# Kernel tuning notes

Hardware: AMD Instinct MI355X
Metric: run time of the kernel (lower is better)

## Reference

```python
import jax, jax.numpy as jnp
import numpy as np

N_NODES = 50000
N_EDGES = 800000
N_GRAPHS = 1024
BN_EPS = 1e-5

def _linear_params(key, fan_in, fan_out):
    k1, k2 = jax.random.split(key)
    lim = 1.0 / np.sqrt(fan_in)
    w = jax.random.uniform(k1, (fan_in, fan_out), jnp.float32, -lim, lim)
    b = jax.random.uniform(k2, (fan_out,), jnp.float32, -lim, lim)
    return w, b


def setup_inputs() -> dict:
    key = jax.random.key(0)
    ks = jax.random.split(key, 16)
    x = jax.random.normal(ks[0], (N_NODES, 114), jnp.float32)
    edge_index = jax.random.randint(ks[1], (2, N_EDGES), 0, N_NODES, jnp.int64)
    batch = jnp.sort(jax.random.randint(ks[2], (N_NODES,), 0, N_GRAPHS, jnp.int64))
    w1a, b1a = _linear_params(ks[3], 114, 198)
    w1b, b1b = _linear_params(ks[4], 198, 198)
    w2a, b2a = _linear_params(ks[5], 198, 64)
    w2b, b2b = _linear_params(ks[6], 64, 64)
    w3a, b3a = _linear_params(ks[7], 64, 32)
    w3b, b3b = _linear_params(ks[8], 32, 32)
    fw1, fb1 = _linear_params(ks[9], 32, 16)
    fw2, fb2 = _linear_params(ks[10], 16, 8)
    ow, ob = _linear_params(ks[11], 8, 2)
    g1 = jnp.ones((198,), jnp.float32); be1 = jnp.zeros((198,), jnp.float32)
    g2 = jnp.ones((64,), jnp.float32); be2 = jnp.zeros((64,), jnp.float32)
    g3 = jnp.ones((32,), jnp.float32); be3 = jnp.zeros((32,), jnp.float32)
    return dict(x=x, edge_index=edge_index, batch=batch,
                w1a=w1a, b1a=b1a, w1b=w1b, b1b=b1b, g1=g1, be1=be1,
                w2a=w2a, b2a=b2a, w2b=w2b, b2b=b2b, g2=g2, be2=be2,
                w3a=w3a, b3a=b3a, w3b=w3b, b3b=b3b, g3=g3, be3=be3,
                fw1=fw1, fb1=fb1, fw2=fw2, fb2=fb2, ow=ow, ob=ob)


def _gin_conv(x, src, dst, wa, ba, wb, bb):
    # GINConv, eps=0: h_i = MLP((1+eps)*x_i + sum_{j->i} x_j)
    agg = jax.ops.segment_sum(x[src], dst, num_segments=N_NODES)
    h = x + agg
    h = jax.nn.relu(h @ wa + ba) @ wb + bb
    return h


def _batchnorm(h, gamma, beta):
    # training-mode BN over the node axis (biased variance, as torch)
    mean = jnp.mean(h, axis=0)
    var = jnp.var(h, axis=0)
    return (h - mean) * jax.lax.rsqrt(var + BN_EPS) * gamma + beta


def reference(x, edge_index, batch,
              w1a, b1a, w1b, b1b, g1, be1,
              w2a, b2a, w2b, b2b, g2, be2,
              w3a, b3a, w3b, b3b, g3, be3,
              fw1, fb1, fw2, fb2, ow, ob):
    src, dst = edge_index[0], edge_index[1]
    h = jax.nn.relu(_gin_conv(x, src, dst, w1a, b1a, w1b, b1b))
    h = _batchnorm(h, g1, be1)
    h = jax.nn.relu(_gin_conv(h, src, dst, w2a, b2a, w2b, b2b))
    h = _batchnorm(h, g2, be2)
    h = jax.nn.relu(_gin_conv(h, src, dst, w3a, b3a, w3b, b3b))
    h = _batchnorm(h, g3, be3)
    g = jax.ops.segment_sum(h, batch, num_segments=N_GRAPHS)  # global_add_pool
    g = jax.nn.relu(g @ fw1 + fb1)
    g = jax.nn.relu(g @ fw2 + fb2)
    return g @ ow + ob
```

## Files before the change

kernel.cpp:

```cpp
#include <hip/hip_runtime.h>

#define NODES  50000
#define EDGES  800000
#define GRAPHS 1024
#define P      200

#define SCAN_BLK 256
#define SCAN_NB  ((NODES + SCAN_BLK - 1) / SCAN_BLK)

typedef __attribute__((ext_vector_type(8))) short short8v;
typedef __attribute__((ext_vector_type(4))) short short4v;
typedef __attribute__((ext_vector_type(4))) float f32x4;

__device__ __forceinline__ ushort f2bf(float f) {
    uint u = __float_as_uint(f);
    u = u + 0x7FFFu + ((u >> 16) & 1u);
    return (ushort)(u >> 16);
}

__global__ void hist_kernel(const int* __restrict__ dst, int* __restrict__ deg,
                            const int* __restrict__ batch, int* __restrict__ cnt) {
    int e = blockIdx.x * blockDim.x + threadIdx.x;
    if (e < EDGES) atomicAdd(&deg[dst[e]], 1);
    if (e < NODES) atomicAdd(&cnt[batch[e]], 1);
}

__global__ void scan_part(const int* __restrict__ deg, int* __restrict__ part) {
    __shared__ int sh[SCAN_BLK];
    int t = threadIdx.x;
    int n = blockIdx.x * SCAN_BLK + t;
    sh[t] = (n < NODES) ? deg[n] : 0;
    __syncthreads();
    for (int off = SCAN_BLK / 2; off > 0; off >>= 1) {
        if (t < off) sh[t] += sh[t + off];
        __syncthreads();
    }
    if (t == 0) part[blockIdx.x] = sh[0];
}

__global__ void scan_scan(int* __restrict__ part) {
    __shared__ int sh[SCAN_BLK];
    int t = threadIdx.x;
    int v = (t < SCAN_NB) ? part[t] : 0;
    sh[t] = v;
    __syncthreads();
    for (int off = 1; off < SCAN_BLK; off <<= 1) {
        int u = 0;
        if (t >= off) u = sh[t - off];
        __syncthreads();
        if (t >= off) sh[t] += u;
        __syncthreads();
    }
    if (t < SCAN_NB) part[t] = sh[t] - v;
}

__global__ void scan_expand(const int* __restrict__ deg, const int* __restrict__ part,
                            int* __restrict__ rowstart, int* __restrict__ cursor) {
    __shared__ int sh[SCAN_BLK];
    int t = threadIdx.x;
    int n = blockIdx.x * SCAN_BLK + t;
    int v = (n < NODES) ? deg[n] : 0;
    sh[t] = v;
    __syncthreads();
    for (int off = 1; off < SCAN_BLK; off <<= 1) {
        int u = 0;
        if (t >= off) u = sh[t - off];
        __syncthreads();
        if (t >= off) sh[t] += u;
        __syncthreads();
    }
    int excl = sh[t] - v + part[blockIdx.x];
    if (n < NODES) {
        rowstart[n] = excl;
        cursor[n]   = excl;
        if (n == NODES - 1) rowstart[NODES] = excl + v;
    }
}

__global__ void scatter_kernel(const int* __restrict__ src, const int* __restrict__ dst,
                               int* __restrict__ cursor, int* __restrict__ csrc) {
    int e = blockIdx.x * blockDim.x + threadIdx.x;
    if (e < EDGES) {
        int p = atomicAdd(&cursor[dst[e]], 1);
        csrc[p] = src[e];
    }
}

__global__ void pad_all(const float* __restrict__ w1a, const float* __restrict__ w1b,
                        const float* __restrict__ w2a, const float* __restrict__ w2b,
                        const float* __restrict__ w3a, const float* __restrict__ w3b,
                        ushort* __restrict__ WF1, ushort* __restrict__ WF2,
                        ushort* __restrict__ WF3, ushort* __restrict__ WF4,
                        ushort* __restrict__ WF5, ushort* __restrict__ WF6) {
    int s = blockIdx.x * blockDim.x + threadIdx.x;
    const float* W; ushort* out; int K, N, NCH, CT, base;
    if      (s < 65536)  { W = w1a; out = WF1; K = 114; N = 198; NCH = 4; CT = 16; base = 0; }
    else if (s < 180224) { W = w1b; out = WF2; K = 198; N = 198; NCH = 7; CT = 16; base = 65536; }
    else if (s < 208896) { W = w2a; out = WF3; K = 198; N = 64;  NCH = 7; CT = 4;  base = 180224; }
    else if (s < 217088) { W = w2b; out = WF4; K = 64;  N = 64;  NCH = 2; CT = 4;  base = 208896; }
    else if (s < 225280) { W = w3a; out = WF5; K = 64;  N = 32;  NCH = 2; CT = 4;  base = 217088; }
    else if (s < 229376) { W = w3b; out = WF6; K = 32;  N = 32;  NCH = 1; CT = 4;  base = 225280; }
    else return;
    int idx = s - base;
    int half = NCH * CT * 512;
    int h = idx / half, r = idx % half;
    int j = r & 7, col = (r >> 3) & 15, kg = (r >> 7) & 3;
    int rest = r >> 9;
    int ct = rest % CT, c = rest / CT;
    int k = c * 32 + kg * 8 + j;
    int n = ct * 16 + col;
    float v = (k < K && n < N) ? W[k * N + n] : 0.0f;
    ushort hi = f2bf(v);
    if (h == 0) out[idx] = hi;
    else {
        float hf = __uint_as_float(((uint)hi) << 16);
        out[idx] = f2bf(v - hf);
    }
}

template<int D>
__global__ void csr_agg(const float* __restrict__ feat, int fpitch,
                        const int* __restrict__ rowstart, const int* __restrict__ csrc,
                        float* __restrict__ agg, int opitch) {
    int wid  = (blockIdx.x * blockDim.x + threadIdx.x) >> 6;
    int lane = threadIdx.x & 63;
    if (wid >= NODES) return;
    const int r0 = rowstart[wid], r1 = rowstart[wid + 1];
    constexpr int UNR = 8;
    if constexpr (D == 114) {
        const bool act = lane < 57;
        float sx = 0.0f, sy = 0.0f;
        for (int base = r0; base < r1; base += 64) {
            const int myidx = (base + lane < r1) ? csrc[base + lane] : 0;
            const int cnt = min(64, r1 - base);
            int t = 0;
            for (; t + UNR <= cnt; t += UNR) {
                const float2* p[UNR];
#pragma unroll
                for (int u = 0; u < UNR; u++)
                    p[u] = (const float2*)(feat + (size_t)__shfl(myidx, t + u) * fpitch);
                float2 v[UNR];
#pragma unroll
                for (int u = 0; u < UNR; u++) if (act) v[u] = p[u][lane];
                if (act) {
                    float ax = 0.0f, ay = 0.0f;
#pragma unroll
                    for (int u = 0; u < UNR; u++) { ax += v[u].x; ay += v[u].y; }
                    sx += ax; sy += ay;
                }
            }
            for (; t < cnt; t++) {
                const float2* fp2 = (const float2*)(feat + (size_t)__shfl(myidx, t) * fpitch);
                if (act) { float2 v = fp2[lane]; sx += v.x; sy += v.y; }
            }
        }
        if (act) *(float2*)(agg + (size_t)wid * opitch + 2 * lane) = make_float2(sx, sy);
    } else {
        float s = 0.0f;
        for (int base = r0; base < r1; base += 64) {
            const int myidx = (base + lane < r1) ? csrc[base + lane] : 0;
            const int cnt = min(64, r1 - base);
            int t = 0;
            for (; t + UNR <= cnt; t += UNR) {
                const float* p[UNR];
#pragma unroll
                for (int u = 0; u < UNR; u++)
                    p[u] = feat + (size_t)__shfl(myidx, t + u) * fpitch;
                float v[UNR];
#pragma unroll
                for (int u = 0; u < UNR; u++)
                    if (lane < D) v[u] = p[u][lane];
                if (lane < D) {
                    float acc = 0.0f;
#pragma unroll
                    for (int u = 0; u < UNR; u++) acc += v[u];
                    s += acc;
                }
            }
            for (; t < cnt; t++) {
                const float* fp2 = feat + (size_t)__shfl(myidx, t) * fpitch;
                if (lane < D) s += fp2[lane];
            }
        }
        if (lane < D) agg[(size_t)wid * opitch + lane] = s;
    }
}

__launch_bounds__(256)
__global__ void gemm_fused_l1(const float* __restrict__ X,
                              const float* __restrict__ A2,
                              const ushort* __restrict__ WF1,
                              const float* __restrict__ B1,
                              const ushort* __restrict__ WF2,
                              const float* __restrict__ B2,
                              float* __restrict__ OUT,
                              float* __restrict__ gsum, float* __restrict__ gsq) {
    constexpr int K1   = 114;
    constexpr int NCH1 = 4;
    constexpr int NCH2 = 7;
    constexpr int CT   = 16;
    constexpr int CTW  = 4;
    constexpr int NN   = 198;

    __shared__ __align__(16) ushort A_lds[2][2][2][4][16][8];
    __shared__ __align__(16) ushort M_lds[2][NCH2][2][4][16][8];
    __shared__ float shSum[256];
    __shared__ float shSq [256];

    const int tid  = threadIdx.x;
    const int lane = tid & 63;
    const int wv   = tid >> 6;
    const int node0 = blockIdx.x * 32;

    for (int n = tid; n < 256; n += 256) { shSum[n] = 0.0f; shSq[n] = 0.0f; }

    const int sr  = tid >> 3;
    const int sc4 = (tid & 7) * 4;
    const int skg = sc4 >> 3;
    const int sj0 = sc4 & 7;
    const int gn  = node0 + sr;
    const size_t fstride1 = (size_t)NCH1 * CT * 512;
    const size_t fstride2 = (size_t)NCH2 * CT * 512;

    float xv[4];
    float a2v[4];

    auto loadA = [&](int c) {
        const int k0 = c * 32 + sc4;
#pragma unroll
        for (int j = 0; j < 4; j++) {
            int gk = k0 + j;
            bool ok = (gn < NODES && gk < K1);
            xv[j]  = ok ? X[(size_t)gn * K1 + gk] : 0.0f;
            a2v[j] = ok ? A2[(size_t)gn * P + gk] : 0.0f;
        }
    };
    auto cvtStore = [&](int buf, int c) {
        const int k0 = c * 32 + sc4;
        short4v hv, lv;
#pragma unroll
        for (int j = 0; j < 4; j++) {
            int gk = k0 + j;
            float t = 0.0f;
            if (gn < NODES && gk < K1) t = xv[j] + a2v[j];
            ushort h = f2bf(t);
            float hf = __uint_as_float(((uint)h) << 16);
            ushort l = f2bf(t - hf);
            hv[j] = (short)h; lv[j] = (short)l;
        }
        *(short4v*)&A_lds[buf][0][sr >> 4][skg][sr & 15][sj0] = hv;
        *(short4v*)&A_lds[buf][1][sr >> 4][skg][sr & 15][sj0] = lv;
    };

    f32x4 acc1[2][CTW] = {};
    loadA(0);
    cvtStore(0, 0);
    __syncthreads();

    const int kg = lane >> 4, rw = lane & 15;
#pragma unroll
    for (int c = 0; c < NCH1; c++) {
        const int buf = c & 1;
        if (c + 1 < NCH1) loadA(c + 1);

        short8v ah[2], al[2];
#pragma unroll
        for (int rt = 0; rt < 2; rt++) {
            ah[rt] = *(const short8v*)&A_lds[buf][0][rt][kg][rw][0];
            al[rt] = *(const short8v*)&A_lds[buf][1][rt][kg][rw][0];
        }
        const size_t fb0 = ((size_t)(c * CT + wv * CTW)) * 512 + (size_t)lane * 8;
        short8v wh = *(const short8v*)(WF1 + fb0);
        short8v wl = *(const short8v*)(WF1 + fstride1 + fb0);
#pragma unroll
        for (int t = 0; t < CTW; t++) {
            short8v nwh, nwl;
            if (t + 1 < CTW) {
                const size_t fb = fb0 + (size_t)(t + 1) * 512;
                nwh = *(const short8v*)(WF1 + fb);
                nwl = *(const short8v*)(WF1 + fstride1 + fb);
            }
            __builtin_amdgcn_s_setprio(1);
#pragma unroll
            for (int rt = 0; rt < 2; rt++) {
                acc1[rt][t] = __builtin_amdgcn_mfma_f32_16x16x32_bf16(ah[rt], wh, acc1[rt][t], 0, 0, 0);
                acc1[rt][t] = __builtin_amdgcn_mfma_f32_16x16x32_bf16(al[rt], wh, acc1[rt][t], 0, 0, 0);
                acc1[rt][t] = __builtin_amdgcn_mfma_f32_16x16x32_bf16(ah[rt], wl, acc1[rt][t], 0, 0, 0);
            }
            __builtin_amdgcn_s_setprio(0);
            if (t + 1 < CTW) { wh = nwh; wl = nwl; }
        }
        if (c + 1 < NCH1) cvtStore((c + 1) & 1, c + 1);
        __syncthreads();
    }

    const int mg = lane >> 4, colb = lane & 15;
#pragma unroll
    for (int t = 0; t < CTW; t++) {
        const int ct = wv * CTW + t;
        if (ct >= 14) continue;
        const int n = ct * 16 + colb;
        const float bn = (n < NN) ? B1[n] : 0.0f;
        const int c2 = n >> 5, kg2 = (n >> 3) & 3, j2 = n & 7;
#pragma unroll
        for (int rt = 0; rt < 2; rt++) {
#pragma unroll
            for (int j = 0; j < 4; j++) {
                float vv = fmaxf(acc1[rt][t][j] + bn, 0.0f);
                if (n >= NN) vv = 0.0f;
                ushort h = f2bf(vv);
                float hf = __uint_as_float(((uint)h) << 16);
                ushort l = f2bf(vv - hf);
                int row = mg * 4 + j;
                M_lds[0][c2][rt][kg2][row][j2] = h;
                M_lds[1][c2][rt][kg2][row][j2] = l;
            }
        }
    }
    __syncthreads();

    f32x4 acc2[2][CTW] = {};
#pragma unroll
    for (int c = 0; c < NCH2; c++) {
        short8v ah[2], al[2];
#pragma unroll
        for (int rt = 0; rt < 2; rt++) {
            ah[rt] = *(const short8v*)&M_lds[0][c][rt][kg][rw][0];
            al[rt] = *(const short8v*)&M_lds[1][c][rt][kg][rw][0];
        }
        const size_t fb0 = ((size_t)(c * CT + wv * CTW)) * 512 + (size_t)lane * 8;
        short8v wh = *(const short8v*)(WF2 + fb0);
        short8v wl = *(const short8v*)(WF2 + fstride2 + fb0);
#pragma unroll
        for (int t = 0; t < CTW; t++) {
            short8v nwh, nwl;
            if (t + 1 < CTW) {
                const size_t fb = fb0 + (size_t)(t + 1) * 512;
                nwh = *(const short8v*)(WF2 + fb);
                nwl = *(const short8v*)(WF2 + fstride2 + fb);
            }
            __builtin_amdgcn_s_setprio(1);
#pragma unroll
            for (int rt = 0; rt < 2; rt++) {
                acc2[rt][t] = __builtin_amdgcn_mfma_f32_16x16x32_bf16(ah[rt], wh, acc2[rt][t], 0, 0, 0);
                acc2[rt][t] = __builtin_amdgcn_mfma_f32_16x16x32_bf16(al[rt], wh, acc2[rt][t], 0, 0, 0);
                acc2[rt][t] = __builtin_amdgcn_mfma_f32_16x16x32_bf16(ah[rt], wl, acc2[rt][t], 0, 0, 0);
            }
            __builtin_amdgcn_s_setprio(0);
            if (t + 1 < CTW) { wh = nwh; wl = nwl; }
        }
    }

#pragma unroll
    for (int t = 0; t < CTW; t++) {
        const int ct = wv * CTW + t;
        const int n = ct * 16 + colb;
        const float bn = (n < NN) ? B2[n] : 0.0f;
        float psum = 0.0f, psq = 0.0f;
#pragma unroll
        for (int rt = 0; rt < 2; rt++) {
#pragma unroll
            for (int j = 0; j < 4; j++) {
                int m = node0 + rt * 16 + mg * 4 + j;
                float vv = fmaxf(acc2[rt][t][j] + bn, 0.0f);
                if (m < NODES && n < NN) {
                    OUT[(size_t)m * P + n] = vv;
                    psum += vv; psq += vv * vv;
                }
            }
        }
        if (n < NN) {
            atomicAdd(&shSum[n], psum);
            atomicAdd(&shSq[n], psq);
        }
    }
    __syncthreads();
    for (int n = tid; n < NN; n += 256) {
        atomicAdd(&gsum[n], shSum[n]);
        atomicAdd(&gsq[n], shSq[n]);
    }
}

template<int K, int N, bool ADD2, bool STATS, bool BNX, bool PRE, bool ACT,
         bool WRITE, bool POOL>
__launch_bounds__(256)
__global__ void gemm_mfma(const float* __restrict__ X, int xpitch,
                          const float* __restrict__ A2, int apitch,
                          const ushort* __restrict__ WF,
                          const float* __restrict__ B,
                          const float* __restrict__ PREB,
                          const float* __restrict__ scale, const float* __restrict__ shift,
                          float* __restrict__ OUT, int opitch,
                          float* __restrict__ gsum, float* __restrict__ gsq,
                          const int* __restrict__ batch, float* __restrict__ gpool) {
    constexpr int KP  = ((K + 31) / 32) * 32;
    constexpr int NCH = KP / 32;
    constexpr int NP  = ((N + 63) / 64) * 64;
    constexpr int CT  = NP / 16;
    constexpr int CTW = CT / 4;
    static_assert(CT % 4 == 0, "col tiles must split across 4 waves");

    __shared__ __align__(16) ushort A_lds[2][2][2][4][16][8];
    __shared__ float shSum[STATS ? NP : 4];
    __shared__ float shSq [STATS ? NP : 4];

    const int tid  = threadIdx.x;
    const int lane = tid & 63;
    const int wv   = tid >> 6;
    const int node0 = blockIdx.x * 32;

    if (STATS) {
        for (int n = tid; n < NP; n += 256) { shSum[n] = 0.0f; shSq[n] = 0.0f; }
    }

    f32x4 acc[2][CTW] = {};

    const int sr  = tid >> 3;
    const int sc4 = (tid & 7) * 4;
    const int skg = sc4 >> 3;
    const int sj0 = sc4 & 7;
    const int gn  = node0 + sr;
    const size_t fstride = (size_t)NCH * CT * 512;

    float xvA[4], xvB[4];
    float a2vA[ADD2 ? 4 : 1], a2vB[ADD2 ? 4 : 1];

    auto loadA_A = [&](int c) {
        const int k0 = c * 32 + sc4;
#pragma unroll
        for (int j = 0; j < 4; j++) {
            int gk = k0 + j;
            bool ok = (gn < NODES && gk < K);
            xvA[j] = ok ? X[(size_t)gn * xpitch + gk] : 0.0f;
            if (ADD2) a2vA[j] = ok ? A2[(size_t)gn * apitch + gk] : 0.0f;
        }
    };
    auto loadA_B = [&](int c) {
        const int k0 = c * 32 + sc4;
#pragma unroll
        for (int j = 0; j < 4; j++) {
            int gk = k0 + j;
            bool ok = (gn < NODES && gk < K);
            xvB[j] = ok ? X[(size_t)gn * xpitch + gk] : 0.0f;
            if (ADD2) a2vB[j] = ok ? A2[(size_t)gn * apitch + gk] : 0.0f;
        }
    };
    auto cvtCore = [&](int buf, int c, const float* xv, const float* a2v) {
        const int k0 = c * 32 + sc4;
        short4v hv, lv;
#pragma unroll
        for (int j = 0; j < 4; j++) {
            int gk = k0 + j;
            float t = 0.0f;
            if (gn < NODES && gk < K) {
                t = xv[j];
                if (BNX) t = fmaf(t, scale[gk], shift[gk]);
                if (ADD2) t += a2v[j];
                if (PRE)  t = fmaxf(t + PREB[gk], 0.0f);
            }
            ushort h = f2bf(t);
            float hf = __uint_as_float(((uint)h) << 16);
            ushort l = f2bf(t - hf);
            hv[j] = (short)h; lv[j] = (short)l;
        }
        *(short4v*)&A_lds[buf][0][sr >> 4][skg][sr & 15][sj0] = hv;
        *(short4v*)&A_lds[buf][1][sr >> 4][skg][sr & 15][sj0] = lv;
    };

    loadA_A(0);
    if (NCH > 1) loadA_B(1);
    cvtCore(0, 0, xvA, ADD2 ? a2vA : xvA);
    __syncthreads();

    const int kg = lane >> 4, rw = lane & 15;
#pragma unroll
    for (int c = 0; c < NCH; c++) {
        const int buf = c & 1;
        if (c + 2 < NCH) {
            if ((c & 1) == 0) loadA_A(c + 2);
            else              loadA_B(c + 2);
        }

        short8v ah[2], al[2];
#pragma unroll
        for (int rt = 0; rt < 2; rt++) {
            ah[rt] = *(const short8v*)&A_lds[buf][0][rt][kg][rw][0];
            al[rt] = *(const short8v*)&A_lds[buf][1][rt][kg][rw][0];
        }

        const size_t fb0 = ((size_t)(c * CT + wv * CTW)) * 512 + (size_t)lane * 8;
        short8v wh = *(const short8v*)(WF + fb0);
        short8v wl = *(const short8v*)(WF + fstride + fb0);
#pragma unroll
        for (int t = 0; t < CTW; t++) {
            short8v nwh, nwl;
            if (t + 1 < CTW) {
                const size_t fb = fb0 + (size_t)(t + 1) * 512;
                nwh = *(const short8v*)(WF + fb);
                nwl = *(const short8v*)(WF + fstride + fb);
            }
            __builtin_amdgcn_s_setprio(1);
#pragma unroll
            for (int rt = 0; rt < 2; rt++) {
                acc[rt][t] = __builtin_amdgcn_mfma_f32_16x16x32_bf16(ah[rt], wh, acc[rt][t], 0, 0, 0);
                acc[rt][t] = __builtin_amdgcn_mfma_f32_16x16x32_bf16(al[rt], wh, acc[rt][t], 0, 0, 0);
                acc[rt][t] = __builtin_amdgcn_mfma_f32_16x16x32_bf16(ah[rt], wl, acc[rt][t], 0, 0, 0);
            }
            __builtin_amdgcn_s_setprio(0);
            if (t + 1 < CTW) { wh = nwh; wl = nwl; }
        }

        if (c + 1 < NCH) {
            if (((c + 1) & 1) == 0) cvtCore((c + 1) & 1, c + 1, xvA, ADD2 ? a2vA : xvA);
            else                    cvtCore((c + 1) & 1, c + 1, xvB, ADD2 ? a2vB : xvB);
        }
        __syncthreads();
    }

    const int mg = lane >> 4, colb = lane & 15;
#pragma unroll
    for (int t = 0; t < CTW; t++) {
        const int ct = wv * CTW + t;
        const int n = ct * 16 + colb;
        const float bn = (ACT && n < N) ? B[n] : 0.0f;
        float psum = 0.0f, psq = 0.0f;
#pragma unroll
        for (int rt = 0; rt < 2; rt++) {
#pragma unroll
            for (int j = 0; j < 4; j++) {
                int m = node0 + rt * 16 + mg * 4 + j;
                float vv = ACT ? fmaxf(acc[rt][t][j] + bn, 0.0f) : acc[rt][t][j];
                if (m < NODES && n < N) {
                    if (WRITE) OUT[(size_t)m * opitch + n] = vv;
                    if (STATS) { psum += vv; psq += vv * vv; }
                    if (POOL)  atomicAdd(&gpool[batch[m] * 32 + n], vv);
                }
            }
        }
        if (STATS && n < N) {
            atomicAdd(&shSum[n], psum);
            atomicAdd(&shSq[n], psq);
        }
    }
    if (STATS) {
        __syncthreads();
        for (int n = tid; n < N; n += 256) {
            atomicAdd(&gsum[n], shSum[n]);
            atomicAdd(&gsq[n], shSq[n]);
        }
    }
}

template<int N>
__global__ void bn_finalize(const float* __restrict__ sum, const float* __restrict__ sq,
                            const float* __restrict__ gamma, const float* __restrict__ beta,
                            float* __restrict__ scale, float* __restrict__ shift) {
    int n = threadIdx.x;
    if (n < N) {
        float mean = sum[n] * (1.0f / NODES);
        float var  = sq[n] * (1.0f / NODES) - mean * mean;
        var = var < 0.0f ? 0.0f : var;
        float sc = gamma[n] * rsqrtf(var + 1e-5f);
        scale[n] = sc;
        shift[n] = beta[n] - mean * sc;
    }
}

__global__ void head_kernel(const float* __restrict__ graw, const int* __restrict__ cnt,
                            const float* __restrict__ scale, const float* __restrict__ shift,
                            const float* __restrict__ fw1, const float* __restrict__ fb1,
                            const float* __restrict__ fw2, const float* __restrict__ fb2,
                            const float* __restrict__ ow, const float* __restrict__ ob,
                            float* __restrict__ out) {
    int gi = blockIdx.x * blockDim.x + threadIdx.x;
    if (gi >= GRAPHS) return;
    float cf = (float)cnt[gi];
    float v[32];
#pragma unroll
    for (int k = 0; k < 32; k++)
        v[k] = fmaf(graw[gi * 32 + k], scale[k], cf * shift[k]);
    float a1[16];
#pragma unroll
    for (int o = 0; o < 16; o++) {
        float s = fb1[o];
#pragma unroll
        for (int k = 0; k < 32; k++) s = fmaf(v[k], fw1[k * 16 + o], s);
        a1[o] = s > 0.0f ? s : 0.0f;
    }
    float a2[8];
#pragma unroll
    for (int o = 0; o < 8; o++) {
        float s = fb2[o];
#pragma unroll
        for (int k = 0; k < 16; k++) s = fmaf(a1[k], fw2[k * 8 + o], s);
        a2[o] = s > 0.0f ? s : 0.0f;
    }
#pragma unroll
    for (int o = 0; o < 2; o++) {
        float s = ob[o];
#pragma unroll
        for (int k = 0; k < 8; k++) s = fmaf(a2[k], ow[k * 2 + o], s);
        out[gi * 2 + o] = s;
    }
}

extern "C" void kernel_launch(void* const* d_in, const int* in_sizes, int n_in,
                              void* d_out, int out_size, void* d_ws, size_t ws_size,
                              hipStream_t stream) {
    const float* x     = (const float*)d_in[0];
    const int*   ei    = (const int*)d_in[1];
    const int*   batch = (const int*)d_in[2];
    const float *w1a = (const float*)d_in[3],  *b1a = (const float*)d_in[4];
    const float *w1b = (const float*)d_in[5],  *b1b = (const float*)d_in[6];
    const float *g1  = (const float*)d_in[7],  *be1 = (const float*)d_in[8];
    const float *w2a = (const float*)d_in[9],  *b2a = (const float*)d_in[10];
    const float *w2b = (const float*)d_in[11], *b2b = (const float*)d_in[12];
    const float *g2  = (const float*)d_in[13], *be2 = (const float*)d_in[14];
    const float *w3a = (const float*)d_in[15], *b3a = (const float*)d_in[16];
    const float *w3b = (const float*)d_in[17], *b3b = (const float*)d_in[18];
    const float *g3  = (const float*)d_in[19], *be3 = (const float*)d_in[20];
    const float *fw1 = (const float*)d_in[21], *fb1 = (const float*)d_in[22];
    const float *fw2 = (const float*)d_in[23], *fb2 = (const float*)d_in[24];
    const float *ow  = (const float*)d_in[25], *ob  = (const float*)d_in[26];
    const int* src = ei;
    const int* dst = ei + EDGES;

    float* ws  = (float*)d_ws;
    float* b0  = ws;
    float* b1  = ws + (size_t)NODES * P;
    float* Y2  = b1;
    float* AG2 = b1 + (size_t)NODES * 64;
    float* Y3  = b1;
    float* AG3 = b1 + (size_t)NODES * 32;

    int*   deg  = (int*)(ws + (size_t)2 * NODES * P);
    int*   cnt  = deg + NODES;
    float* SUM1 = (float*)(cnt + GRAPHS);
    float* SQ1  = SUM1 + 256;
    float* SUM2 = SQ1 + 256;
    float* SQ2  = SUM2 + 256;
    float* SUM3 = SQ2 + 256;
    float* SQ3  = SUM3 + 256;
    float* G    = SQ3 + 256;
    const size_t ZERO_ELEMS = (size_t)NODES + GRAPHS + 6 * 256 + (size_t)GRAPHS * 32;

    float* SCALE = G + (size_t)GRAPHS * 32;
    float* SHIFT = SCALE + 256;
    int* rowstart = (int*)(SHIFT + 256);
    int* cursor   = rowstart + NODES + 1;
    int* part     = cursor + NODES;
    int* csrc     = part + 256;
    uintptr_t wfp = ((uintptr_t)(csrc + EDGES) + 15) & ~(uintptr_t)15;
    ushort* WF1 = (ushort*)wfp;
    ushort* WF2 = WF1 + 65536;
    ushort* WF3 = WF2 + 114688;
    ushort* WF4 = WF3 + 28672;
    ushort* WF5 = WF4 + 8192;
    ushort* WF6 = WF5 + 8192;
    float* out = (float*)d_out;

    const int GBR = (NODES + 31) / 32;
    const int AB = (NODES * 64 + 255) / 256;
    const int EB = (EDGES + 255) / 256;

    pad_all<<<(229376 + 255) / 256, 256, 0, stream>>>(w1a, w1b, w2a, w2b, w3a, w3b,
                                                      WF1, WF2, WF3, WF4, WF5, WF6);
    hipMemsetAsync(deg, 0, ZERO_ELEMS * sizeof(int), stream);

    hist_kernel<<<EB, 256, 0, stream>>>(dst, deg, batch, cnt);
    scan_part<<<SCAN_NB, SCAN_BLK, 0, stream>>>(deg, part);
    scan_scan<<<1, SCAN_BLK, 0, stream>>>(part);
    scan_expand<<<SCAN_NB, SCAN_BLK, 0, stream>>>(deg, part, rowstart, cursor);
    scatter_kernel<<<EB, 256, 0, stream>>>(src, dst, cursor, csrc);

    csr_agg<114><<<AB, 256, 0, stream>>>(x, 114, rowstart, csrc, b0, P);
    gemm_fused_l1<<<GBR, 256, 0, stream>>>(x, b0, WF1, b1a, WF2, b1b, b0, SUM1, SQ1);
    bn_finalize<198><<<1, 256, 0, stream>>>(SUM1, SQ1, g1, be1, SCALE, SHIFT);

    gemm_mfma<198, 64, false, false, true, false, false, true, false><<<GBR, 256, 0, stream>>>(
        b0, P, nullptr, 0, WF3, nullptr, nullptr, SCALE, SHIFT, Y2, 64, nullptr, nullptr,
        nullptr, nullptr);
    csr_agg<64><<<AB, 256, 0, stream>>>(Y2, 64, rowstart, csrc, AG2, 64);
    gemm_mfma<64, 64, true, true, false, true, true, true, false><<<GBR, 256, 0, stream>>>(
        Y2, 64, AG2, 64, WF4, b2b, b2a, nullptr, nullptr, b0, 64, SUM2, SQ2,
        nullptr, nullptr);
    bn_finalize<64><<<1, 256, 0, stream>>>(SUM2, SQ2, g2, be2, SCALE, SHIFT);

    gemm_mfma<64, 32, false, false, true, false, false, true, false><<<GBR, 256, 0, stream>>>(
        b0, 64, nullptr, 0, WF5, nullptr, nullptr, SCALE, SHIFT, Y3, 32, nullptr, nullptr,
        nullptr, nullptr);
    csr_agg<32><<<AB, 256, 0, stream>>>(Y3, 32, rowstart, csrc, AG3, 32);
    gemm_mfma<32, 32, true, true, false, true, true, false, true><<<GBR, 256, 0, stream>>>(
        Y3, 32, AG3, 32, WF6, b3b, b3a, nullptr, nullptr, nullptr, 32, SUM3, SQ3,
        batch, G);
    bn_finalize<32><<<1, 256, 0, stream>>>(SUM3, SQ3, g3, be3, SCALE, SHIFT);

    head_kernel<<<(GRAPHS + 255) / 256, 256, 0, stream>>>(
        G, cnt, SCALE, SHIFT, fw1, fb1, fw2, fb2, ow, ob, out);
}
```

Before: 436.9 us.

## Fold BN finalize into consumer kernels and pack two nodes per wave in 32-wide aggregation

Removes the three single-block bn_finalize launches. Each consumer GEMM block now computes BN scale and shift into shared memory from the raw sums, and the head kernel computes them per thread. Separately, the 32-feature CSR aggregation now handles two nodes per 64-lane wave, using half-waves, so lanes no longer sit idle and the grid is halved. The cost is redundant per-block BN math and an extra block-level barrier in the GEMM.

```diff
diff --git a/kernel.cpp b/kernel.cpp
--- a/kernel.cpp
+++ b/kernel.cpp
@@ -124,10 +124,40 @@
                         float* __restrict__ agg, int opitch) {
     int wid  = (blockIdx.x * blockDim.x + threadIdx.x) >> 6;
     int lane = threadIdx.x & 63;
-    if (wid >= NODES) return;
-    const int r0 = rowstart[wid], r1 = rowstart[wid + 1];
     constexpr int UNR = 8;
-    if constexpr (D == 114) {
+    if constexpr (D == 32) {
+        const int half = lane >> 5, sub = lane & 31;
+        const int node = 2 * wid + half;
+        const bool nact = node < NODES;
+        const int r0 = nact ? rowstart[node] : 0;
+        const int r1 = nact ? rowstart[node + 1] : 0;
+        float s = 0.0f;
+        for (int base = r0; base < r1; base += 32) {
+            const int myidx = (base + sub < r1) ? csrc[base + sub] : 0;
+            const int cnt = min(32, r1 - base);
+            int t = 0;
+            for (; t + UNR <= cnt; t += UNR) {
+                const float* p[UNR];
+#pragma unroll
+                for (int u = 0; u < UNR; u++)
+                    p[u] = feat + (size_t)__shfl(myidx, 32 * half + t + u) * fpitch;
+                float v[UNR];
+#pragma unroll
+                for (int u = 0; u < UNR; u++) v[u] = p[u][sub];
+                float acc = 0.0f;
+#pragma unroll
+                for (int u = 0; u < UNR; u++) acc += v[u];
+                s += acc;
+            }
+            for (; t < cnt; t++) {
+                const float* fp2 = feat + (size_t)__shfl(myidx, 32 * half + t) * fpitch;
+                s += fp2[sub];
+            }
+        }
+        if (nact) agg[(size_t)node * opitch + sub] = s;
+    } else if constexpr (D == 114) {
+        if (wid >= NODES) return;
+        const int r0 = rowstart[wid], r1 = rowstart[wid + 1];
         const bool act = lane < 57;
         float sx = 0.0f, sy = 0.0f;
         for (int base = r0; base < r1; base += 64) {
@@ -156,6 +186,8 @@
         }
         if (act) *(float2*)(agg + (size_t)wid * opitch + 2 * lane) = make_float2(sx, sy);
     } else {
+        if (wid >= NODES) return;
+        const int r0 = rowstart[wid], r1 = rowstart[wid + 1];
         float s = 0.0f;
         for (int base = r0; base < r1; base += 64) {
             const int myidx = (base + lane < r1) ? csrc[base + lane] : 0;
@@ -389,7 +421,8 @@
                           const ushort* __restrict__ WF,
                           const float* __restrict__ B,
                           const float* __restrict__ PREB,
-                          const float* __restrict__ scale, const float* __restrict__ shift,
+                          const float* __restrict__ bnsum, const float* __restrict__ bnsq,
+                          const float* __restrict__ gamma, const float* __restrict__ beta,
                           float* __restrict__ OUT, int opitch,
                           float* __restrict__ gsum, float* __restrict__ gsq,
                           const int* __restrict__ batch, float* __restrict__ gpool) {
@@ -403,6 +436,8 @@
     __shared__ __align__(16) ushort A_lds[2][2][2][4][16][8];
     __shared__ float shSum[STATS ? NP : 4];
     __shared__ float shSq [STATS ? NP : 4];
+    __shared__ float shSc [BNX ? 256 : 4];
+    __shared__ float shSh [BNX ? 256 : 4];
 
     const int tid  = threadIdx.x;
     const int lane = tid & 63;
@@ -411,6 +446,17 @@
 
     if (STATS) {
         for (int n = tid; n < NP; n += 256) { shSum[n] = 0.0f; shSq[n] = 0.0f; }
+    }
+    if (BNX) {
+        if (tid < K) {
+            float mean = bnsum[tid] * (1.0f / NODES);
+            float var  = bnsq[tid] * (1.0f / NODES) - mean * mean;
+            var = var < 0.0f ? 0.0f : var;
+            float sc = gamma[tid] * rsqrtf(var + 1e-5f);
+            shSc[tid] = sc;
+            shSh[tid] = beta[tid] - mean * sc;
+        }
+        __syncthreads();
     }
 
     f32x4 acc[2][CTW] = {};
@@ -454,7 +500,7 @@
             float t = 0.0f;
             if (gn < NODES && gk < K) {
                 t = xv[j];
-                if (BNX) t = fmaf(t, scale[gk], shift[gk]);
+                if (BNX) t = fmaf(t, shSc[gk], shSh[gk]);
                 if (ADD2) t += a2v[j];
                 if (PRE)  t = fmaxf(t + PREB[gk], 0.0f);
             }
@@ -551,23 +597,9 @@
     }
 }
 
-template<int N>
-__global__ void bn_finalize(const float* __restrict__ sum, const float* __restrict__ sq,
+__global__ void head_kernel(const float* __restrict__ graw, const int* __restrict__ cnt,
+                            const float* __restrict__ bnsum, const float* __restrict__ bnsq,
                             const float* __restrict__ gamma, const float* __restrict__ beta,
-                            float* __restrict__ scale, float* __restrict__ shift) {
-    int n = threadIdx.x;
-    if (n < N) {
-        float mean = sum[n] * (1.0f / NODES);
-        float var  = sq[n] * (1.0f / NODES) - mean * mean;
-        var = var < 0.0f ? 0.0f : var;
-        float sc = gamma[n] * rsqrtf(var + 1e-5f);
-        scale[n] = sc;
-        shift[n] = beta[n] - mean * sc;
-    }
-}
-
-__global__ void head_kernel(const float* __restrict__ graw, const int* __restrict__ cnt,
-                            const float* __restrict__ scale, const float* __restrict__ shift,
                             const float* __restrict__ fw1, const float* __restrict__ fb1,
                             const float* __restrict__ fw2, const float* __restrict__ fb2,
                             const float* __restrict__ ow, const float* __restrict__ ob,
@@ -577,8 +609,14 @@
     float cf = (float)cnt[gi];
     float v[32];
 #pragma unroll
-    for (int k = 0; k < 32; k++)
-        v[k] = fmaf(graw[gi * 32 + k], scale[k], cf * shift[k]);
+    for (int k = 0; k < 32; k++) {
+        float mean = bnsum[k] * (1.0f / NODES);
+        float var  = bnsq[k] * (1.0f / NODES) - mean * mean;
+        var = var < 0.0f ? 0.0f : var;
+        float sc = gamma[k] * rsqrtf(var + 1e-5f);
+        float sh = beta[k] - mean * sc;
+        v[k] = fmaf(graw[gi * 32 + k], sc, cf * sh);
+    }
     float a1[16];
 #pragma unroll
     for (int o = 0; o < 16; o++) {
@@ -644,9 +682,7 @@
     float* G    = SQ3 + 256;
     const size_t ZERO_ELEMS = (size_t)NODES + GRAPHS + 6 * 256 + (size_t)GRAPHS * 32;
 
-    float* SCALE = G + (size_t)GRAPHS * 32;
-    float* SHIFT = SCALE + 256;
-    int* rowstart = (int*)(SHIFT + 256);
+    int* rowstart = (int*)(G + (size_t)GRAPHS * 32);
     int* cursor   = rowstart + NODES + 1;
     int* part     = cursor + NODES;
     int* csrc     = part + 256;
@@ -659,9 +695,10 @@
     ushort* WF6 = WF5 + 8192;
     float* out = (float*)d_out;
 
-    const int GBR = (NODES + 31) / 32;
-    const int AB = (NODES * 64 + 255) / 256;
-    const int EB = (EDGES + 255) / 256;
+    const int GBR  = (NODES + 31) / 32;
+    const int AB   = (NODES * 64 + 255) / 256;
+    const int AB2  = (((NODES + 1) / 2) * 64 + 255) / 256;
+    const int EB   = (EDGES + 255) / 256;
 
     pad_all<<<(229376 + 255) / 256, 256, 0, stream>>>(w1a, w1b, w2a, w2b, w3a, w3b,
                                                       WF1, WF2, WF3, WF4, WF5, WF6);
@@ -675,26 +712,23 @@
 
     csr_agg<114><<<AB, 256, 0, stream>>>(x, 114, rowstart, csrc, b0, P);
     gemm_fused_l1<<<GBR, 256, 0, stream>>>(x, b0, WF1, b1a, WF2, b1b, b0, SUM1, SQ1);
-    bn_finalize<198><<<1, 256, 0, stream>>>(SUM1, SQ1, g1, be1, SCALE, SHIFT);
 
     gemm_mfma<198, 64, false, false, true, false, false, true, false><<<GBR, 256, 0, stream>>>(
-        b0, P, nullptr, 0, WF3, nullptr, nullptr, SCALE, SHIFT, Y2, 64, nullptr, nullptr,
-        nullptr, nullptr);
+        b0, P, nullptr, 0, WF3, nullptr, nullptr, SUM1, SQ1, g1, be1,
+        Y2, 64, nullptr, nullptr, nullptr, nullptr);
     csr_agg<64><<<AB, 256, 0, stream>>>(Y2, 64, rowstart, csrc, AG2, 64);
     gemm_mfma<64, 64, true, true, false, true, true, true, false><<<GBR, 256, 0, stream>>>(
-        Y2, 64, AG2, 64, WF4, b2b, b2a, nullptr, nullptr, b0, 64, SUM2, SQ2,
-        nullptr, nullptr);
-    bn_finalize<64><<<1, 256, 0, stream>>>(SUM2, SQ2, g2, be2, SCALE, SHIFT);
+        Y2, 64, AG2, 64, WF4, b2b, b2a, nullptr, nullptr, nullptr, nullptr,
+        b0, 64, SUM2, SQ2, nullptr, nullptr);
 
     gemm_mfma<64, 32, false, false, true, false, false, true, false><<<GBR, 256, 0, stream>>>(
-        b0, 64, nullptr, 0, WF5, nullptr, nullptr, SCALE, SHIFT, Y3, 32, nullptr, nullptr,
-        nullptr, nullptr);
-    csr_agg<32><<<AB, 256, 0, stream>>>(Y3, 32, rowstart, csrc, AG3, 32);
+        b0, 64, nullptr, 0, WF5, nullptr, nullptr, SUM2, SQ2, g2, be2,
+        Y3, 32, nullptr, nullptr, nullptr, nullptr);
+    csr_agg<32><<<AB2, 256, 0, stream>>>(Y3, 32, rowstart, csrc, AG3, 32);
     gemm_mfma<32, 32, true, true, false, true, true, false, true><<<GBR, 256, 0, stream>>>(
-        Y3, 32, AG3, 32, WF6, b3b, b3a, nullptr, nullptr, nullptr, 32, SUM3, SQ3,
-        batch, G);
-    bn_finalize<32><<<1, 256, 0, stream>>>(SUM3, SQ3, g3, be3, SCALE, SHIFT);
+        Y3, 32, AG3, 32, WF6, b3b, b3a, nullptr, nullptr, nullptr, nullptr,
+        nullptr, 32, SUM3, SQ3, batch, G);
 
     head_kernel<<<(GRAPHS + 255) / 256, 256, 0, stream>>>(
-        G, cnt, SCALE, SHIFT, fw1, fb1, fw2, fb2, ow, ob, out);
-}
+        G, cnt, SUM3, SQ3, g3, be3, fw1, fb1, fw2, fb2, ow, ob, out);
+}
```

Result: faster. 413.8 us (-5.3%).
